# Kernel tuning notes

Measured on AMD Instinct MI355X. Metric: run time of the kernel, lower is better.

## Reference

```python
import jax, jax.numpy as jnp
import numpy as np

DIM = 128
RES = 64
H_SP, W_SP = 64, 4   # idx == 0: H_sp = resolution, W_sp = split_size
NUM_HEADS = 4
HEAD_DIM = DIM // NUM_HEADS
SCALE = HEAD_DIM ** -0.5


def img2windows(img, H_sp, W_sp):
    # img: (B, C, H, W) -> (B*nHw*nWw, H_sp*W_sp, C)
    B, C, H, W = img.shape
    x = img.reshape(B, C, H // H_sp, H_sp, W // W_sp, W_sp)
    x = jnp.transpose(x, (0, 2, 4, 3, 5, 1))
    return x.reshape(-1, H_sp * W_sp, C)


def windows2img(wins, H_sp, W_sp, H, W):
    C = wins.shape[-1]
    B = wins.shape[0] // ((H // H_sp) * (W // W_sp))
    x = wins.reshape(B, H // H_sp, W // W_sp, H_sp, W_sp, C)
    x = jnp.transpose(x, (0, 5, 1, 3, 2, 4))
    return x.reshape(B, C, H, W)


def im2cswin(x, H_sp, W_sp, num_heads):
    # (B, C, H, W) -> (B', num_heads, L, head_dim)
    C = x.shape[1]
    w = img2windows(x, H_sp, W_sp)                       # (B', L, C)
    w = w.reshape(-1, H_sp * W_sp, num_heads, C // num_heads)
    return jnp.transpose(w, (0, 2, 1, 3))


def conv1x1(x, w, b):
    # x: (B, C, H, W), w: (O, C), b: (O,)
    return jnp.einsum('bchw,oc->bohw', x, w) + b[None, :, None, None]


def depthwise5x5(x, w, b):
    # x: (B, C, H, W), w: (C, 1, 5, 5) depthwise, pad=2
    y = jax.lax.conv_general_dilated(
        x, w, window_strides=(1, 1), padding=((2, 2), (2, 2)),
        feature_group_count=x.shape[1],
        dimension_numbers=('NCHW', 'OIHW', 'NCHW'))
    return y + b[None, :, None, None]


def setup_inputs() -> dict:
    key = jax.random.key(0)
    ks = jax.random.split(key, 8)
    B = 16
    x = jax.random.normal(ks[0], (B, DIM, RES, RES), dtype=jnp.float32)
    n_windows = B * (RES // H_SP) * (RES // W_SP)
    L = H_SP * W_SP
    attn_input = jax.random.normal(ks[1], (n_windows, NUM_HEADS, L, L), dtype=jnp.float32)
    s = 0.02
    wq = jax.random.normal(ks[2], (DIM, DIM), dtype=jnp.float32) * s
    bq = jnp.zeros((DIM,), dtype=jnp.float32)
    wv = jax.random.normal(ks[3], (DIM, DIM), dtype=jnp.float32) * s
    bv = jnp.zeros((DIM,), dtype=jnp.float32)
    w_lepe = jax.random.normal(ks[4], (DIM, 1, 5, 5), dtype=jnp.float32) * s
    b_lepe = jnp.zeros((DIM,), dtype=jnp.float32)
    temperature = jnp.ones((NUM_HEADS, 1, 1), dtype=jnp.float32)
    return {"x": x, "attn_input": attn_input, "wq": wq, "bq": bq,
            "wv": wv, "bv": bv, "w_lepe": w_lepe, "b_lepe": b_lepe,
            "temperature": temperature}


def reference(x, attn_input, wq, bq, wv, bv, w_lepe, b_lepe, temperature):
    B, C, H, W = x.shape
    v_map = conv1x1(x, wv, bv)
    lepe = depthwise5x5(v_map, w_lepe, b_lepe)           # (B, C, H, W)
    # shift_size == 0: no roll
    q_map = conv1x1(x, wq, bq)
    q = im2cswin(q_map + lepe, H_SP, W_SP, NUM_HEADS) * SCALE  # (B', nh, L, d)
    k = im2cswin(x + lepe, H_SP, W_SP, NUM_HEADS)
    v = im2cswin(v_map, H_SP, W_SP, NUM_HEADS)
    scores = jnp.einsum('whqd,whkd->whqk', q, k)         # (B', nh, L, L)
    attn = jax.nn.softmax(scores, axis=-1) + temperature[None] * attn_input
    out = jnp.einsum('whqk,whkd->whqd', attn, v)         # (B', nh, L, d)
    out = jnp.transpose(out, (0, 2, 1, 3)).reshape(-1, H_SP * W_SP, C)
    out = windows2img(out, H_SP, W_SP, H, W)             # (B, C, H, W)
    return (out + lepe, attn)
```

## Files before the change

kernel.cpp:

```cpp
#include <hip/hip_runtime.h>

typedef __attribute__((ext_vector_type(4)))  float fx4;
typedef __attribute__((ext_vector_type(16))) float fx16;
typedef __attribute__((ext_vector_type(8)))  short bf8;
typedef __attribute__((ext_vector_type(4)))  unsigned int u32x4;

#define SCALE 0.17677669529663687f

__device__ __forceinline__ unsigned short f2bf(float f) {
  unsigned int u = __builtin_bit_cast(unsigned int, f);
  unsigned int r = (u + 0x7fffu + ((u >> 16) & 1u)) >> 16;
  return (unsigned short)r;
}
__device__ __forceinline__ float bf2f(unsigned short u) {
  unsigned int v = ((unsigned int)u) << 16;
  return __builtin_bit_cast(float, v);
}

__global__ __launch_bounds__(256) void k0_xT(const float* __restrict__ x,
                                             unsigned short* __restrict__ xT) {
  int h = blockIdx.x, b = blockIdx.y, t = threadIdx.x;
  __shared__ unsigned short tile[128 * 68];
  const float* xrow = x + ((size_t)b * 128 * 4096) + h * 64;
#pragma unroll
  for (int i = 0; i < 8; ++i) {
    int slot = t + i * 256;
    int c = slot >> 4, wq = slot & 15;
    float4 v = *reinterpret_cast<const float4*>(xrow + (size_t)c * 4096 + wq * 4);
    unsigned short* p = &tile[c * 68 + wq * 4];
    p[0] = f2bf(v.x); p[1] = f2bf(v.y); p[2] = f2bf(v.z); p[3] = f2bf(v.w);
  }
  __syncthreads();
  int w = t >> 2, cc = t & 3;
  unsigned short tmp[32];
#pragma unroll
  for (int j = 0; j < 32; ++j) tmp[j] = tile[(cc * 32 + j) * 68 + w];
  unsigned short* dst = xT + ((size_t)(b * 4096 + h * 64 + w)) * 128 + cc * 32;
#pragma unroll
  for (int q = 0; q < 4; ++q)
    *reinterpret_cast<bf8*>(dst + q * 8) = *reinterpret_cast<bf8*>(tmp + q * 8);
}

__global__ __launch_bounds__(256) void k1_conv(const unsigned short* __restrict__ xT,
    const float* __restrict__ wq, const float* __restrict__ bq,
    const float* __restrict__ wv, const float* __restrict__ bv,
    unsigned short* __restrict__ qT, unsigned short* __restrict__ vT) {
  int pt = blockIdx.x, b = blockIdx.y, qv = blockIdx.z;
  const float* W = qv ? wv : wq;
  const float* bias = qv ? bv : bq;
  unsigned short* out = qv ? vT : qT;
  int t = threadIdx.x, lane = t & 63, wave = t >> 6;
  int wm = wave >> 1, wn = wave & 1;
  int l31 = lane & 31, g2 = lane >> 5;
  fx16 acc[2][2] = {};
  const unsigned short* Abase = xT + ((size_t)b * 4096 + pt * 128) * 128;
#pragma unroll
  for (int ks = 0; ks < 8; ++ks) {
    int kbase = ks * 16 + g2 * 8;
    bf8 a[2], bb[2];
#pragma unroll
    for (int mi = 0; mi < 2; ++mi) {
      int pix = (wm * 2 + mi) * 32 + l31;
      a[mi] = *reinterpret_cast<const bf8*>(Abase + (size_t)pix * 128 + kbase);
    }
#pragma unroll
    for (int ni = 0; ni < 2; ++ni) {
      int oc = (wn * 2 + ni) * 32 + l31;
      const float* wp = W + oc * 128 + kbase;
      float4 w0 = *reinterpret_cast<const float4*>(wp);
      float4 w1 = *reinterpret_cast<const float4*>(wp + 4);
      bf8 r;
      r[0]=(short)f2bf(w0.x); r[1]=(short)f2bf(w0.y); r[2]=(short)f2bf(w0.z); r[3]=(short)f2bf(w0.w);
      r[4]=(short)f2bf(w1.x); r[5]=(short)f2bf(w1.y); r[6]=(short)f2bf(w1.z); r[7]=(short)f2bf(w1.w);
      bb[ni] = r;
    }
#pragma unroll
    for (int mi = 0; mi < 2; ++mi)
#pragma unroll
      for (int ni = 0; ni < 2; ++ni)
        acc[mi][ni] = __builtin_amdgcn_mfma_f32_32x32x16_bf16(a[mi], bb[ni], acc[mi][ni], 0, 0, 0);
  }
#pragma unroll
  for (int ni = 0; ni < 2; ++ni) {
    int oc = (wn * 2 + ni) * 32 + l31;
    float bsv = bias[oc];
#pragma unroll
    for (int mi = 0; mi < 2; ++mi) {
#pragma unroll
      for (int r = 0; r < 16; ++r) {
        int row = (r & 3) + 8 * (r >> 2) + 4 * g2;
        int pix = pt * 128 + (wm * 2 + mi) * 32 + row;
        out[((size_t)b * 4096 + pix) * 128 + oc] = f2bf(acc[mi][ni][r] + bsv);
      }
    }
  }
}

__global__ __launch_bounds__(256) void k2_lepe(const unsigned short* __restrict__ vT,
    const float* __restrict__ wl5, const float* __restrict__ bl,
    unsigned short* __restrict__ lepe,
    unsigned short* __restrict__ kT_io, unsigned short* __restrict__ qT_io) {
  int strip = blockIdx.x, hd = blockIdx.y, b = blockIdx.z;
  int t = threadIdx.x;
  __shared__ unsigned short tile[12 * 64 * 34];
  int h0 = strip * 8;
#pragma unroll
  for (int i = 0; i < 12; ++i) {
    int slot = t + i * 256;
    int r = slot >> 8;
    int rem = slot & 255;
    int w = rem >> 2, cc = rem & 3;
    int h = h0 - 2 + r;
    unsigned short vv[8];
    if (h >= 0 && h < 64) {
      *reinterpret_cast<bf8*>(vv) = *reinterpret_cast<const bf8*>(
          vT + ((size_t)b * 4096 + h * 64 + w) * 128 + hd * 32 + cc * 8);
    } else {
#pragma unroll
      for (int j = 0; j < 8; ++j) vv[j] = 0;
    }
    unsigned int* dst = reinterpret_cast<unsigned int*>(&tile[(r * 64 + w) * 34 + cc * 8]);
#pragma unroll
    for (int j = 0; j < 4; ++j)
      dst[j] = ((unsigned int)vv[2 * j + 1] << 16) | (unsigned int)vv[2 * j];
  }
  __syncthreads();
  int c2 = t & 15, w16 = t >> 4;
  int c = c2 * 2;
  float wt0[25], wt1[25];
#pragma unroll
  for (int i = 0; i < 25; ++i) {
    wt0[i] = wl5[(hd * 32 + c) * 25 + i];
    wt1[i] = wl5[(hd * 32 + c + 1) * 25 + i];
  }
  float b0 = bl[hd * 32 + c], b1 = bl[hd * 32 + c + 1];
  for (int hh = 0; hh < 8; ++hh) {
    for (int wi = 0; wi < 4; ++wi) {
      int w = w16 * 4 + wi;
      float a0 = b0, a1 = b1;
#pragma unroll
      for (int dy = 0; dy < 5; ++dy) {
        int rr = hh + dy;
#pragma unroll
        for (int dx = 0; dx < 5; ++dx) {
          int wx = w + dx - 2;
          if (wx < 0 || wx >= 64) continue;
          unsigned int pr = *reinterpret_cast<const unsigned int*>(&tile[(rr * 64 + wx) * 34 + c]);
          float v0 = bf2f((unsigned short)(pr & 0xffffu));
          float v1 = bf2f((unsigned short)(pr >> 16));
          a0 += v0 * wt0[dy * 5 + dx];
          a1 += v1 * wt1[dy * 5 + dx];
        }
      }
      size_t po = ((size_t)b * 4096 + (h0 + hh) * 64 + w) * 128 + hd * 32 + c;
      unsigned int lp = (unsigned int)f2bf(a0) | ((unsigned int)f2bf(a1) << 16);
      *reinterpret_cast<unsigned int*>(&lepe[po]) = lp;
      unsigned int kx = *reinterpret_cast<const unsigned int*>(&kT_io[po]);
      unsigned int qx = *reinterpret_cast<const unsigned int*>(&qT_io[po]);
      unsigned int kn = (unsigned int)f2bf(bf2f((unsigned short)(kx & 0xffffu)) + a0)
                      | ((unsigned int)f2bf(bf2f((unsigned short)(kx >> 16)) + a1) << 16);
      unsigned int qn = (unsigned int)f2bf((bf2f((unsigned short)(qx & 0xffffu)) + a0) * SCALE)
                      | ((unsigned int)f2bf((bf2f((unsigned short)(qx >> 16)) + a1) * SCALE) << 16);
      *reinterpret_cast<unsigned int*>(&kT_io[po]) = kn;
      *reinterpret_cast<unsigned int*>(&qT_io[po]) = qn;
    }
  }
}

__global__ __launch_bounds__(256, 4) void k3_attn(
    const unsigned short* __restrict__ kT, const unsigned short* __restrict__ qS,
    const unsigned short* __restrict__ vT,
    const float* __restrict__ ai, const float* __restrict__ temp,
    float* __restrict__ attn, unsigned short* __restrict__ out_win) {
  int w = blockIdx.x;
  int hd = blockIdx.y;
  int b = w >> 4, ww = w & 15;
  int t = threadIdx.x, lane = t & 63, wave = t >> 6;
  int l15 = lane & 15, g = (lane >> 4) & 3;
  __shared__ unsigned short Kf[16 * 4 * 16 * 8];
  __shared__ unsigned short Vf[16 * 4 * 16 * 8];
  __shared__ float Stg[4 * 512];

  const size_t aBase = ((size_t)w * 4 + hd) * 65536;
  const float* aiB = ai + aBase;
  float* atB = attn + aBase;
  unsigned short* owB = out_win + ((size_t)w * 4 + hd) * 8192;

  fx4 av[8];
  {
    int qrow0 = wave * 16 + l15;
    const fx4* aiRow0 = reinterpret_cast<const fx4*>(aiB + (size_t)qrow0 * 256 + g * 4);
#pragma unroll
    for (int nt = 0; nt < 8; ++nt) av[nt] = aiRow0[nt * 4];
  }
  asm volatile("" ::: "memory");

  {
    int row = t;
    int pix = (row >> 2) * 64 + ww * 4 + (row & 3);
    const unsigned short* src = kT + ((size_t)b * 4096 + pix) * 128 + hd * 32;
    int nt = row >> 4, sl = row & 15;
#pragma unroll
    for (int gg = 0; gg < 4; ++gg)
      *reinterpret_cast<bf8*>(&Kf[((nt * 4 + gg) * 16 + sl) * 8]) =
          *reinterpret_cast<const bf8*>(src + gg * 8);
  }
  {
    int row = t;
    int pix = (row >> 2) * 64 + ww * 4 + (row & 3);
    const unsigned short* src = vT + ((size_t)b * 4096 + pix) * 128 + hd * 32;
    unsigned short vv[32];
#pragma unroll
    for (int q = 0; q < 4; ++q)
      *reinterpret_cast<bf8*>(vv + q * 8) = *reinterpret_cast<const bf8*>(src + q * 8);
    int ks = row >> 5, gg = (row >> 3) & 3, j = row & 7;
#pragma unroll
    for (int d = 0; d < 32; ++d)
      Vf[(((ks * 2 + (d >> 4)) * 4 + gg) * 16 + (d & 15)) * 8 + j] = vv[d];
  }
  __syncthreads();
  float tHd = temp[hd];

  int srcA = l15 + ((lane & 16) << 1);
  int srcB = srcA + 16;
  bool ghi = (lane >= 32);
  float* Sw = Stg + wave * 512;

  for (int pass = 0; pass < 4; ++pass) {
    int qbase = (pass * 4 + wave) * 16;
    int qrow = qbase + l15;
    const fx4* aiRow = reinterpret_cast<const fx4*>(aiB + (size_t)qrow * 256 + g * 4);

    bf8 qf;
    {
      int pix = (qrow >> 2) * 64 + ww * 4 + (qrow & 3);
      qf = *reinterpret_cast<const bf8*>(
          qS + ((size_t)b * 4096 + pix) * 128 + hd * 32 + g * 8);
    }

    fx4 acc[16];
#pragma unroll
    for (int nt = 0; nt < 16; ++nt) {
      bf8 kfr = *reinterpret_cast<const bf8*>(&Kf[((nt * 4 + g) * 16 + l15) * 8]);
      fx4 z; z[0] = 0.f; z[1] = 0.f; z[2] = 0.f; z[3] = 0.f;
      acc[nt] = __builtin_amdgcn_mfma_f32_16x16x32_bf16(kfr, qf, z, 0, 0, 0);
    }

    float m0 = fmaxf(acc[0][0], acc[0][1]), m1 = fmaxf(acc[0][2], acc[0][3]);
    float m2 = fmaxf(acc[1][0], acc[1][1]), m3 = fmaxf(acc[1][2], acc[1][3]);
#pragma unroll
    for (int nt = 2; nt < 16; nt += 2) {
      m0 = fmaxf(m0, fmaxf(acc[nt][0], acc[nt][1]));
      m1 = fmaxf(m1, fmaxf(acc[nt][2], acc[nt][3]));
      m2 = fmaxf(m2, fmaxf(acc[nt + 1][0], acc[nt + 1][1]));
      m3 = fmaxf(m3, fmaxf(acc[nt + 1][2], acc[nt + 1][3]));
    }
    float m = fmaxf(fmaxf(m0, m1), fmaxf(m2, m3));
    m = fmaxf(m, __shfl_xor(m, 16));
    m = fmaxf(m, __shfl_xor(m, 32));

    float s0 = 0.f, s1 = 0.f, s2 = 0.f, s3 = 0.f;
#pragma unroll
    for (int nt = 0; nt < 16; ++nt) {
      float p0 = __expf(acc[nt][0] - m);
      float p1 = __expf(acc[nt][1] - m);
      float p2 = __expf(acc[nt][2] - m);
      float p3 = __expf(acc[nt][3] - m);
      acc[nt][0] = p0; acc[nt][1] = p1; acc[nt][2] = p2; acc[nt][3] = p3;
      s0 += p0; s1 += p1; s2 += p2; s3 += p3;
    }
    float s = (s0 + s1) + (s2 + s3);
    s += __shfl_xor(s, 16);
    s += __shfl_xor(s, 32);
    float inv = 1.0f / s;

    fx4 av2[8];
#pragma unroll
    for (int nt = 0; nt < 8; ++nt) av2[nt] = aiRow[(8 + nt) * 4];
    asm volatile("" ::: "memory");

    unsigned int pp0[16], pp1[16];
#pragma unroll
    for (int p = 0; p < 8; ++p) {
#pragma unroll
      for (int u = 0; u < 2; ++u) {
        int nt = 2 * p + u;
        fx4 a4 = (nt < 8) ? av[nt] : av2[nt - 8];
        fx4 sv;
        sv[0] = acc[nt][0] * inv + tHd * a4[0];
        sv[1] = acc[nt][1] * inv + tHd * a4[1];
        sv[2] = acc[nt][2] * inv + tHd * a4[2];
        sv[3] = acc[nt][3] * inv + tHd * a4[3];
        int pc = (g + 4 * u) ^ (l15 & 7);
        *reinterpret_cast<fx4*>(&Sw[l15 * 32 + pc * 4]) = sv;
        pp0[nt] = (unsigned int)f2bf(sv[0]) | ((unsigned int)f2bf(sv[1]) << 16);
        pp1[nt] = (unsigned int)f2bf(sv[2]) | ((unsigned int)f2bf(sv[3]) << 16);
      }
#pragma unroll
      for (int i = 0; i < 2; ++i) {
        int r = (lane >> 3) + 8 * i;
        int cf = lane & 7;
        int pc = cf ^ (r & 7);
        fx4 v = *reinterpret_cast<const fx4*>(&Sw[r * 32 + pc * 4]);
        __builtin_nontemporal_store(v,
            reinterpret_cast<fx4*>(atB + (size_t)(qbase + r) * 256 + p * 32 + cf * 4));
      }
    }

    if (pass < 3) {
      int qrowN = ((pass + 1) * 4 + wave) * 16 + l15;
      const fx4* aiRowN = reinterpret_cast<const fx4*>(aiB + (size_t)qrowN * 256 + g * 4);
#pragma unroll
      for (int nt = 0; nt < 8; ++nt) av[nt] = aiRowN[nt * 4];
      asm volatile("" ::: "memory");
    }

    fx4 oT[2];
    oT[0][0]=0.f;oT[0][1]=0.f;oT[0][2]=0.f;oT[0][3]=0.f;
    oT[1][0]=0.f;oT[1][1]=0.f;oT[1][2]=0.f;oT[1][3]=0.f;
#pragma unroll
    for (int c = 0; c < 8; ++c) {
      int n0 = 2 * c, n1 = 2 * c + 1;
      unsigned int x0 = (unsigned int)__shfl((int)pp0[n0], srcA);
      unsigned int y0 = (unsigned int)__shfl((int)pp0[n1], srcA);
      unsigned int x1 = (unsigned int)__shfl((int)pp1[n0], srcA);
      unsigned int y1 = (unsigned int)__shfl((int)pp1[n1], srcA);
      unsigned int x2 = (unsigned int)__shfl((int)pp0[n0], srcB);
      unsigned int y2 = (unsigned int)__shfl((int)pp0[n1], srcB);
      unsigned int x3 = (unsigned int)__shfl((int)pp1[n0], srcB);
      unsigned int y3 = (unsigned int)__shfl((int)pp1[n1], srcB);
      u32x4 bw;
      bw[0] = ghi ? y0 : x0;
      bw[1] = ghi ? y1 : x1;
      bw[2] = ghi ? y2 : x2;
      bw[3] = ghi ? y3 : x3;
      bf8 pf = __builtin_bit_cast(bf8, bw);
#pragma unroll
      for (int dblk = 0; dblk < 2; ++dblk) {
        bf8 vf = *reinterpret_cast<const bf8*>(&Vf[(((c * 2 + dblk) * 4 + g) * 16 + l15) * 8]);
        oT[dblk] = __builtin_amdgcn_mfma_f32_16x16x32_bf16(vf, pf, oT[dblk], 0, 0, 0);
      }
    }
#pragma unroll
    for (int dblk = 0; dblk < 2; ++dblk) {
      unsigned int w0 = (unsigned int)f2bf(oT[dblk][0]) | ((unsigned int)f2bf(oT[dblk][1]) << 16);
      unsigned int w1 = (unsigned int)f2bf(oT[dblk][2]) | ((unsigned int)f2bf(oT[dblk][3]) << 16);
      uint2 st; st.x = w0; st.y = w1;
      *reinterpret_cast<uint2*>(&owB[(size_t)qrow * 32 + dblk * 16 + g * 4]) = st;
    }
  }
}

__global__ __launch_bounds__(256) void k4_out(const unsigned short* __restrict__ out_win,
    const unsigned short* __restrict__ lepe, float* __restrict__ out0) {
  int h = blockIdx.x, b = blockIdx.y, t = threadIdx.x;
  __shared__ float winb[16 * 533];
  __shared__ float lep[64 * 129];
#pragma unroll
  for (int i = 0; i < 4; ++i) {
    int slot = t + i * 256;
    int ww = slot >> 6, rem = slot & 63;
    int hdq = rem >> 4, rem2 = rem & 15;
    int wl = rem2 >> 2, dq = rem2 & 3;
    bf8 v = *reinterpret_cast<const bf8*>(
        out_win + (((size_t)(b * 16 + ww) * 4 + hdq) * 256 + h * 4 + wl) * 32 + dq * 8);
    float* p = &winb[ww * 533 + wl * 133 + hdq * 33 + dq * 8];
#pragma unroll
    for (int j = 0; j < 8; ++j) p[j] = bf2f((unsigned short)v[j]);
  }
#pragma unroll
  for (int i = 0; i < 4; ++i) {
    int slot = t + i * 256;
    int w = slot >> 4, cq = slot & 15;
    bf8 lv = *reinterpret_cast<const bf8*>(
        lepe + ((size_t)b * 4096 + h * 64 + w) * 128 + cq * 8);
    float* p = &lep[w * 129 + cq * 8];
#pragma unroll
    for (int j = 0; j < 8; ++j) p[j] = bf2f((unsigned short)lv[j]);
  }
  __syncthreads();
  int w = t & 63, cg = t >> 6;
#pragma unroll
  for (int ci = 0; ci < 32; ++ci) {
    int c = cg * 32 + ci;
    float val = winb[(w >> 2) * 533 + (w & 3) * 133 + (c >> 5) * 33 + (c & 31)] + lep[w * 129 + c];
    out0[((size_t)(b * 128 + c) * 64 + h) * 64 + w] = val;
  }
}

extern "C" void kernel_launch(void* const* d_in, const int* in_sizes, int n_in,
                              void* d_out, int out_size, void* d_ws, size_t ws_size,
                              hipStream_t stream) {
  const float* x    = (const float*)d_in[0];
  const float* ai   = (const float*)d_in[1];
  const float* wq   = (const float*)d_in[2];
  const float* bq   = (const float*)d_in[3];
  const float* wv   = (const float*)d_in[4];
  const float* bv   = (const float*)d_in[5];
  const float* wl5  = (const float*)d_in[6];
  const float* bl   = (const float*)d_in[7];
  const float* temp = (const float*)d_in[8];
  float* out0 = (float*)d_out;
  float* attn = out0 + 8388608;

  char* ws = (char*)d_ws;
  unsigned short* xT = (unsigned short*)(ws);
  unsigned short* qT = (unsigned short*)(ws + 16777216);
  unsigned short* vT = (unsigned short*)(ws + 33554432);
  unsigned short* lepe = (unsigned short*)(ws + 50331648);
  unsigned short* ow = (unsigned short*)(ws + 83886080);

  k0_xT  <<<dim3(64, 16),    256, 0, stream>>>(x, xT);
  k1_conv<<<dim3(32, 16, 2), 256, 0, stream>>>(xT, wq, bq, wv, bv, qT, vT);
  k2_lepe<<<dim3(8, 4, 16),  256, 0, stream>>>(vT, wl5, bl, lepe, xT, qT);
  k3_attn<<<dim3(256, 4),    256, 0, stream>>>(xT, qT, vT, ai, temp, attn, ow);
  k4_out <<<dim3(64, 16),    256, 0, stream>>>(ow, lepe, out0);
}
```

Measured before the change: 255.1 us.

## Fuse x transpose/bf16 conversion into the Q/V 1x1 conv kernel

Merges the transpose kernel and the 1x1 conv kernel into one. Each block loads a 128-pixel x 128-channel tile of x into shared memory as bf16, writes xT out for later kernels, and computes both Q and V projections from LDS instead of reading xT from global memory. This removes a launch and a global round trip for the conv's A operand. In exchange the grid is halved (no qv dimension), so there is less parallelism, and the LDS tile is larger.

```diff
diff --git a/kernel.cpp b/kernel.cpp
--- a/kernel.cpp
+++ b/kernel.cpp
@@ -17,80 +17,80 @@
   return __builtin_bit_cast(float, v);
 }
 
-__global__ __launch_bounds__(256) void k0_xT(const float* __restrict__ x,
-                                             unsigned short* __restrict__ xT) {
-  int h = blockIdx.x, b = blockIdx.y, t = threadIdx.x;
-  __shared__ unsigned short tile[128 * 68];
-  const float* xrow = x + ((size_t)b * 128 * 4096) + h * 64;
-#pragma unroll
-  for (int i = 0; i < 8; ++i) {
-    int slot = t + i * 256;
-    int c = slot >> 4, wq = slot & 15;
-    float4 v = *reinterpret_cast<const float4*>(xrow + (size_t)c * 4096 + wq * 4);
-    unsigned short* p = &tile[c * 68 + wq * 4];
-    p[0] = f2bf(v.x); p[1] = f2bf(v.y); p[2] = f2bf(v.z); p[3] = f2bf(v.w);
-  }
-  __syncthreads();
-  int w = t >> 2, cc = t & 3;
-  unsigned short tmp[32];
-#pragma unroll
-  for (int j = 0; j < 32; ++j) tmp[j] = tile[(cc * 32 + j) * 68 + w];
-  unsigned short* dst = xT + ((size_t)(b * 4096 + h * 64 + w)) * 128 + cc * 32;
-#pragma unroll
-  for (int q = 0; q < 4; ++q)
-    *reinterpret_cast<bf8*>(dst + q * 8) = *reinterpret_cast<bf8*>(tmp + q * 8);
-}
-
-__global__ __launch_bounds__(256) void k1_conv(const unsigned short* __restrict__ xT,
+__global__ __launch_bounds__(256) void k01_qv(const float* __restrict__ x,
     const float* __restrict__ wq, const float* __restrict__ bq,
     const float* __restrict__ wv, const float* __restrict__ bv,
-    unsigned short* __restrict__ qT, unsigned short* __restrict__ vT) {
-  int pt = blockIdx.x, b = blockIdx.y, qv = blockIdx.z;
-  const float* W = qv ? wv : wq;
-  const float* bias = qv ? bv : bq;
-  unsigned short* out = qv ? vT : qT;
-  int t = threadIdx.x, lane = t & 63, wave = t >> 6;
+    unsigned short* __restrict__ xT, unsigned short* __restrict__ qT,
+    unsigned short* __restrict__ vT) {
+  int pt = blockIdx.x, b = blockIdx.y, t = threadIdx.x;
+  __shared__ unsigned short tT[128 * 136];
+  const float* xb = x + (size_t)b * 524288 + pt * 128;
+#pragma unroll
+  for (int i = 0; i < 16; ++i) {
+    int slot = t + i * 256;
+    int c = slot >> 5, p4 = slot & 31;
+    float4 v = *reinterpret_cast<const float4*>(xb + (size_t)c * 4096 + p4 * 4);
+    unsigned short* q = &tT[(p4 * 4) * 136 + c];
+    q[0] = f2bf(v.x); q[136] = f2bf(v.y); q[272] = f2bf(v.z); q[408] = f2bf(v.w);
+  }
+  __syncthreads();
+  {
+    int pix = t >> 1, hf = t & 1;
+    unsigned short tmp[64];
+#pragma unroll
+    for (int j = 0; j < 64; ++j) tmp[j] = tT[pix * 136 + hf * 64 + j];
+    unsigned short* dst = xT + ((size_t)b * 4096 + pt * 128 + pix) * 128 + hf * 64;
+#pragma unroll
+    for (int q = 0; q < 8; ++q)
+      *reinterpret_cast<bf8*>(dst + q * 8) = *reinterpret_cast<bf8*>(tmp + q * 8);
+  }
+  int lane = t & 63, wave = t >> 6;
   int wm = wave >> 1, wn = wave & 1;
   int l31 = lane & 31, g2 = lane >> 5;
-  fx16 acc[2][2] = {};
-  const unsigned short* Abase = xT + ((size_t)b * 4096 + pt * 128) * 128;
-#pragma unroll
-  for (int ks = 0; ks < 8; ++ks) {
-    int kbase = ks * 16 + g2 * 8;
-    bf8 a[2], bb[2];
-#pragma unroll
-    for (int mi = 0; mi < 2; ++mi) {
-      int pix = (wm * 2 + mi) * 32 + l31;
-      a[mi] = *reinterpret_cast<const bf8*>(Abase + (size_t)pix * 128 + kbase);
+#pragma unroll
+  for (int qv = 0; qv < 2; ++qv) {
+    const float* W = qv ? wv : wq;
+    const float* bias = qv ? bv : bq;
+    unsigned short* out = qv ? vT : qT;
+    fx16 acc[2][2] = {};
+#pragma unroll
+    for (int ks = 0; ks < 8; ++ks) {
+      int kbase = ks * 16 + g2 * 8;
+      bf8 a[2], bb[2];
+#pragma unroll
+      for (int mi = 0; mi < 2; ++mi) {
+        int pix = (wm * 2 + mi) * 32 + l31;
+        a[mi] = *reinterpret_cast<const bf8*>(&tT[pix * 136 + kbase]);
+      }
+#pragma unroll
+      for (int ni = 0; ni < 2; ++ni) {
+        int oc = (wn * 2 + ni) * 32 + l31;
+        const float* wp = W + oc * 128 + kbase;
+        float4 w0 = *reinterpret_cast<const float4*>(wp);
+        float4 w1 = *reinterpret_cast<const float4*>(wp + 4);
+        bf8 r;
+        r[0]=(short)f2bf(w0.x); r[1]=(short)f2bf(w0.y); r[2]=(short)f2bf(w0.z); r[3]=(short)f2bf(w0.w);
+        r[4]=(short)f2bf(w1.x); r[5]=(short)f2bf(w1.y); r[6]=(short)f2bf(w1.z); r[7]=(short)f2bf(w1.w);
+        bb[ni] = r;
+      }
+#pragma unroll
+      for (int mi = 0; mi < 2; ++mi)
+#pragma unroll
+        for (int ni = 0; ni < 2; ++ni)
+          acc[mi][ni] = __builtin_amdgcn_mfma_f32_32x32x16_bf16(a[mi], bb[ni], acc[mi][ni], 0, 0, 0);
     }
 #pragma unroll
     for (int ni = 0; ni < 2; ++ni) {
       int oc = (wn * 2 + ni) * 32 + l31;
-      const float* wp = W + oc * 128 + kbase;
-      float4 w0 = *reinterpret_cast<const float4*>(wp);
-      float4 w1 = *reinterpret_cast<const float4*>(wp + 4);
-      bf8 r;
-      r[0]=(short)f2bf(w0.x); r[1]=(short)f2bf(w0.y); r[2]=(short)f2bf(w0.z); r[3]=(short)f2bf(w0.w);
-      r[4]=(short)f2bf(w1.x); r[5]=(short)f2bf(w1.y); r[6]=(short)f2bf(w1.z); r[7]=(short)f2bf(w1.w);
-      bb[ni] = r;
-    }
-#pragma unroll
-    for (int mi = 0; mi < 2; ++mi)
-#pragma unroll
-      for (int ni = 0; ni < 2; ++ni)
-        acc[mi][ni] = __builtin_amdgcn_mfma_f32_32x32x16_bf16(a[mi], bb[ni], acc[mi][ni], 0, 0, 0);
-  }
-#pragma unroll
-  for (int ni = 0; ni < 2; ++ni) {
-    int oc = (wn * 2 + ni) * 32 + l31;
-    float bsv = bias[oc];
-#pragma unroll
-    for (int mi = 0; mi < 2; ++mi) {
-#pragma unroll
-      for (int r = 0; r < 16; ++r) {
-        int row = (r & 3) + 8 * (r >> 2) + 4 * g2;
-        int pix = pt * 128 + (wm * 2 + mi) * 32 + row;
-        out[((size_t)b * 4096 + pix) * 128 + oc] = f2bf(acc[mi][ni][r] + bsv);
+      float bsv = bias[oc];
+#pragma unroll
+      for (int mi = 0; mi < 2; ++mi) {
+#pragma unroll
+        for (int r = 0; r < 16; ++r) {
+          int row = (r & 3) + 8 * (r >> 2) + 4 * g2;
+          int pix = pt * 128 + (wm * 2 + mi) * 32 + row;
+          out[((size_t)b * 4096 + pix) * 128 + oc] = f2bf(acc[mi][ni][r] + bsv);
+        }
       }
     }
   }
@@ -410,9 +410,8 @@
   unsigned short* lepe = (unsigned short*)(ws + 50331648);
   unsigned short* ow = (unsigned short*)(ws + 83886080);
 
-  k0_xT  <<<dim3(64, 16),    256, 0, stream>>>(x, xT);
-  k1_conv<<<dim3(32, 16, 2), 256, 0, stream>>>(xT, wq, bq, wv, bv, qT, vT);
-  k2_lepe<<<dim3(8, 4, 16),  256, 0, stream>>>(vT, wl5, bl, lepe, xT, qT);
-  k3_attn<<<dim3(256, 4),    256, 0, stream>>>(xT, qT, vT, ai, temp, attn, ow);
-  k4_out <<<dim3(64, 16),    256, 0, stream>>>(ow, lepe, out0);
-}
+  k01_qv <<<dim3(32, 16),   256, 0, stream>>>(x, wq, bq, wv, bv, xT, qT, vT);
+  k2_lepe<<<dim3(8, 4, 16), 256, 0, stream>>>(vT, wl5, bl, lepe, xT, qT);
+  k3_attn<<<dim3(256, 4),   256, 0, stream>>>(xT, qT, vT, ai, temp, attn, ow);
+  k4_out <<<dim3(64, 16),   256, 0, stream>>>(ow, lepe, out0);
+}
```

Result: no change. 250.3 us (-1.9%).
